# Performance work log

Measured on AMD Instinct MI355X. Metric: run time of the kernel, lower is better.

Reference implementation:

```python
import jax, jax.numpy as jnp
import numpy as np

B, T = 16, 1024
EMBED, HIDDEN = 128, 256
NUM_CLASSES, NUM_LABELS = 8000, 100


def setup_inputs() -> dict:
    key = jax.random.key(0)
    ks = jax.random.split(key, 9)
    s_in = 1.0 / np.sqrt(HIDDEN)  # PyTorch LSTMCell init: U(-1/sqrt(H), 1/sqrt(H))
    return {
        "x": jax.random.randint(ks[0], (B, T, 2), 0, NUM_LABELS, dtype=jnp.int64),
        "embed_x_w": jax.random.uniform(ks[1], (NUM_CLASSES, EMBED), jnp.float32, -0.1, 0.1),
        "embed_label_w": jax.random.uniform(ks[2], (NUM_LABELS, EMBED), jnp.float32, -0.1, 0.1),
        "W_ih": jax.random.uniform(ks[3], (4 * HIDDEN, 2 * EMBED), jnp.float32, -s_in, s_in),
        "W_hh": jax.random.uniform(ks[4], (4 * HIDDEN, HIDDEN), jnp.float32, -s_in, s_in),
        "b_ih": jax.random.uniform(ks[5], (4 * HIDDEN,), jnp.float32, -s_in, s_in),
        "b_hh": jax.random.uniform(ks[6], (4 * HIDDEN,), jnp.float32, -s_in, s_in),
        "fc_w": jax.random.uniform(ks[7], (NUM_CLASSES, HIDDEN), jnp.float32, -s_in, s_in),
        "fc_b": jax.random.uniform(ks[8], (NUM_CLASSES,), jnp.float32, -s_in, s_in),
    }


def _lstm_forward(x, embed_x_w, embed_label_w, W_ih, W_hh, b_ih, b_hh, fc_w, fc_b):
    H = W_hh.shape[1]
    # embedding lookups + concat: [B, T, 2E]
    x_emb = embed_x_w[x[:, :, 0]]
    l_emb = embed_label_w[x[:, :, 1]]
    inp = jnp.concatenate([x_emb, l_emb], axis=-1)
    # precompute input projection for all timesteps: [T, B, 4H]
    x_proj = jnp.einsum("bte,ge->tbg", inp, W_ih) + b_ih + b_hh

    def step(carry, xp_t):
        h, c = carry
        gates = xp_t + h @ W_hh.T  # [B, 4H]
        i = jax.nn.sigmoid(gates[:, 0 * H:1 * H])
        f = jax.nn.sigmoid(gates[:, 1 * H:2 * H])
        g = jnp.tanh(gates[:, 2 * H:3 * H])
        o = jax.nn.sigmoid(gates[:, 3 * H:4 * H])
        c_new = f * c + i * g
        h_new = o * jnp.tanh(c_new)
        return (h_new, c_new), h_new

    bsz = x.shape[0]
    h0 = jnp.zeros((bsz, H), x_proj.dtype)
    c0 = jnp.zeros((bsz, H), x_proj.dtype)
    _, hs = jax.lax.scan(step, (h0, c0), x_proj)  # hs: [T, B, H]
    hs = jnp.transpose(hs, (1, 0, 2))  # [B, T, H]
    return jnp.einsum("bth,ch->btc", hs, fc_w) + fc_b  # [B, T, C]


def reference(x, embed_x_w, embed_label_w, W_ih, W_hh, b_ih, b_hh, fc_w, fc_b):
    return _lstm_forward(x, embed_x_w, embed_label_w, W_ih, W_hh, b_ih, b_hh, fc_w, fc_b)
```

## Files before the change

kernel.cpp:

```cpp
#include <hip/hip_runtime.h>
#include <hip/hip_bf16.h>
#include <stdint.h>

#define B_ 16
#define T_ 1024
#define EMBED_ 128
#define HID_ 256
#define G4_ 1024
#define NC_ 8000
#define M_ (B_*T_)

typedef short bf16x8 __attribute__((ext_vector_type(8)));
typedef float f32x4 __attribute__((ext_vector_type(4)));

#if defined(__has_builtin)
#if __has_builtin(__builtin_amdgcn_sdot4)
#define SDOT4(a,b,c) __builtin_amdgcn_sdot4((a),(b),(c),false)
#endif
#endif
#ifndef SDOT4
__device__ __forceinline__ int sdot4_sw(int a, int b, int c) {
    c += (int)(signed char)(a)       * (int)(signed char)(b);
    c += (int)(signed char)(a >> 8)  * (int)(signed char)(b >> 8);
    c += (int)(signed char)(a >> 16) * (int)(signed char)(b >> 16);
    c += (int)(signed char)(a >> 24) * (int)(signed char)(b >> 24);
    return c;
}
#define SDOT4(a,b,c) sdot4_sw((a),(b),(c))
#endif

__device__ __forceinline__ float sigmoid_f(float x) {
    float e = __expf(-x);
    return __builtin_amdgcn_rcpf(1.f + e);
}

__global__ void embed_kernel(const int* __restrict__ x,
                             const float* __restrict__ ew,
                             const float* __restrict__ lw,
                             __hip_bfloat16* __restrict__ inp) {
    int m = blockIdx.x;
    int e = threadIdx.x;
    int i0 = x[2 * m];
    int i1 = x[2 * m + 1];
    float v = (e < EMBED_) ? ew[i0 * EMBED_ + e] : lw[i1 * EMBED_ + (e - EMBED_)];
    inp[m * 256 + e] = __float2bfloat16(v);
}

__global__ void f2bf_kernel(const float* __restrict__ in,
                            __hip_bfloat16* __restrict__ out, int n) {
    int i = blockIdx.x * blockDim.x + threadIdx.x;
    if (i < n) out[i] = __float2bfloat16(in[i]);
}

__global__ void quant_whh_kernel(const float* __restrict__ whh,
                                 int* __restrict__ wq, float* __restrict__ wscale) {
    int r = blockIdx.x;
    int lane = threadIdx.x;
    float4 v = ((const float4*)(whh + r * HID_))[lane];
    float m = fmaxf(fmaxf(fabsf(v.x), fabsf(v.y)), fmaxf(fabsf(v.z), fabsf(v.w)));
    #pragma unroll
    for (int off = 32; off; off >>= 1) m = fmaxf(m, __shfl_xor(m, off, 64));
    m = fmaxf(m, 1e-20f);
    float inv = 127.f / m;
    int q0 = __float2int_rn(v.x * inv) & 255;
    int q1 = __float2int_rn(v.y * inv) & 255;
    int q2 = __float2int_rn(v.z * inv) & 255;
    int q3 = __float2int_rn(v.w * inv) & 255;
    wq[r * 64 + lane] = q0 | (q1 << 8) | (q2 << 16) | (q3 << 24);
    if (lane == 0) wscale[r] = m * (1.f / 127.f);
}

__global__ __launch_bounds__(256, 4)
void gemm_bf16_kernel(const __hip_bfloat16* __restrict__ A,
                      const __hip_bfloat16* __restrict__ Bm,
                      const float* __restrict__ bias1,
                      const float* __restrict__ bias2,
                      float* __restrict__ C,
                      int N, int out_mode) {
    __shared__ short As[64][136];
    __shared__ short Bs[64][136];
    const int tid = threadIdx.x;
    const int m0 = blockIdx.y * 64;
    const int n0 = blockIdx.x * 64;
    const int w = tid >> 6;
    const int lane = tid & 63;
    const int l15 = lane & 15;
    const int q = lane >> 4;

    f32x4 zero4 = {0.f, 0.f, 0.f, 0.f};
    f32x4 acc[4] = {zero4, zero4, zero4, zero4};

    const int r = tid >> 2;
    const int cbase = tid & 3;

    for (int ko = 0; ko < 256; ko += 128) {
        #pragma unroll
        for (int i = 0; i < 4; ++i) {
            int c = cbase + (i << 2);
            uint4 av = ((const uint4*)A)[(size_t)(m0 + r) * 32 + (ko >> 3) + c];
            *((uint4*)&As[r][c * 8]) = av;
            uint4 bv = ((const uint4*)Bm)[(size_t)(n0 + r) * 32 + (ko >> 3) + c];
            *((uint4*)&Bs[r][c * 8]) = bv;
        }
        __syncthreads();
        #pragma unroll
        for (int kc = 0; kc < 4; ++kc) {
            bf16x8 af = *((const bf16x8*)&As[w * 16 + l15][kc * 32 + q * 8]);
            #pragma unroll
            for (int nt = 0; nt < 4; ++nt) {
                bf16x8 bfr = *((const bf16x8*)&Bs[nt * 16 + l15][kc * 32 + q * 8]);
                acc[nt] = __builtin_amdgcn_mfma_f32_16x16x32_bf16(af, bfr, acc[nt], 0, 0, 0);
            }
        }
        __syncthreads();
    }

    #pragma unroll
    for (int nt = 0; nt < 4; ++nt) {
        int n = n0 + nt * 16 + l15;
        float bsum = bias1[n] + (bias2 ? bias2[n] : 0.f);
        #pragma unroll
        for (int rg = 0; rg < 4; ++rg) {
            int m = m0 + w * 16 + q * 4 + rg;
            float val = acc[nt][rg] + bsum;
            if (out_mode == 0) {
                C[(size_t)m * N + n] = val;
            } else {
                int t = m & (T_ - 1), b = m >> 10;
                C[((size_t)((t << 4) + b) << 10) + n] = val;
            }
        }
    }
}

__global__ __launch_bounds__(512, 2)
void lstm_scan_kernel(const int* __restrict__ wq,
                      const float* __restrict__ wscale,
                      const float* __restrict__ xproj,
                      __hip_bfloat16* __restrict__ hs) {
    __shared__ __align__(16) int h_lds[2][64];

    const int tid = threadIdx.x;
    const int b = blockIdx.x;
    const int u = tid >> 1;
    const int odd = tid & 1;
    const int r0 = odd ? (256 + u) : u;
    const int r1 = odd ? (768 + u) : (512 + u);

    int w0[64], w1[64];
    {
        const int4* p0 = (const int4*)wq + r0 * 16;
        const int4* p1 = (const int4*)wq + r1 * 16;
        #pragma unroll
        for (int i = 0; i < 16; ++i) {
            int4 a = p0[i];
            w0[4 * i + 0] = a.x; w0[4 * i + 1] = a.y; w0[4 * i + 2] = a.z; w0[4 * i + 3] = a.w;
            int4 bb = p1[i];
            w1[4 * i + 0] = bb.x; w1[4 * i + 1] = bb.y; w1[4 * i + 2] = bb.z; w1[4 * i + 3] = bb.w;
        }
    }
    const float qs0 = wscale[r0] * (1.f / 127.f);
    const float qs1 = wscale[r1] * (1.f / 127.f);
    const float kb = odd ? 1.f : 2.f;
    const float mb = odd ? 1.f : 2.f;
    const float nb = odd ? 0.f : -1.f;

    if (tid < 64) h_lds[0][tid] = 0;
    float c = 0.f;
    float xp0 = xproj[(b << 10) + r0];
    float xp1 = xproj[(b << 10) + r1];
    __syncthreads();

    for (int t = 0; t < T_; ++t) {
        float nx0 = 0.f, nx1 = 0.f;
        if (t < T_ - 1) {
            const float* p = xproj + ((size_t)(((t + 1) << 4) + b) << 10);
            nx0 = p[r0];
            nx1 = p[r1];
        }
        int acc0 = 0, acc1 = 0;
        const int* hb = h_lds[t & 1];
        #pragma unroll
        for (int kd = 0; kd < 16; ++kd) {
            int4 hv = *((const int4*)(hb + kd * 4));
            acc0 = SDOT4(w0[4 * kd + 0], hv.x, acc0);
            acc0 = SDOT4(w0[4 * kd + 1], hv.y, acc0);
            acc0 = SDOT4(w0[4 * kd + 2], hv.z, acc0);
            acc0 = SDOT4(w0[4 * kd + 3], hv.w, acc0);
            acc1 = SDOT4(w1[4 * kd + 0], hv.x, acc1);
            acc1 = SDOT4(w1[4 * kd + 1], hv.y, acc1);
            acc1 = SDOT4(w1[4 * kd + 2], hv.z, acc1);
            acc1 = SDOT4(w1[4 * kd + 3], hv.w, acc1);
        }
        float ga = (float)acc0 * qs0 + xp0;
        float gb = (float)acc1 * qs1 + xp1;
        float a0 = sigmoid_f(ga);
        float a1 = sigmoid_f(kb * gb) * mb + nb;
        float pa0 = __shfl_xor(a0, 1, 64);
        float pa1 = __shfl_xor(a1, 1, 64);
        float iv = odd ? pa0 : a0;
        float fv = odd ? a0 : pa0;
        float gv = odd ? pa1 : a1;
        float ov = odd ? a1 : pa1;
        c = fv * c + iv * gv;
        float th = 2.f * sigmoid_f(c + c) - 1.f;
        float h = ov * th;
        if (!odd) {
            hs[(((size_t)(b << 10) + t) << 8) + u] = __float2bfloat16(h);
            ((signed char*)h_lds[(t + 1) & 1])[u] =
                (signed char)__float2int_rn(h * 127.f);
        }
        asm volatile("s_waitcnt lgkmcnt(0)" ::: "memory");
        __builtin_amdgcn_s_barrier();
        __builtin_amdgcn_sched_barrier(0);
        xp0 = nx0;
        xp1 = nx1;
    }
}

extern "C" void kernel_launch(void* const* d_in, const int* in_sizes, int n_in,
                              void* d_out, int out_size, void* d_ws, size_t ws_size,
                              hipStream_t stream) {
    const int* x            = (const int*)d_in[0];
    const float* embed_x_w  = (const float*)d_in[1];
    const float* embed_lb_w = (const float*)d_in[2];
    const float* W_ih       = (const float*)d_in[3];
    const float* W_hh       = (const float*)d_in[4];
    const float* b_ih       = (const float*)d_in[5];
    const float* b_hh       = (const float*)d_in[6];
    const float* fc_w       = (const float*)d_in[7];
    const float* fc_b       = (const float*)d_in[8];
    float* out = (float*)d_out;

    char* ws = (char*)d_ws;
    __hip_bfloat16* inp_bf = (__hip_bfloat16*)(ws);
    __hip_bfloat16* wih_bf = (__hip_bfloat16*)(ws + 8388608);
    __hip_bfloat16* fcw_bf = (__hip_bfloat16*)(ws + 8912896);
    int*   whh_q           = (int*)(ws + 13008896);
    float* whh_s           = (float*)(ws + 13271040);
    float* xproj           = (float*)(ws + 13275136);
    __hip_bfloat16* hs     = (__hip_bfloat16*)(ws + 80384000);
    (void)in_sizes; (void)n_in; (void)out_size; (void)ws_size;

    hipLaunchKernelGGL(embed_kernel, dim3(M_), dim3(256), 0, stream,
                       x, embed_x_w, embed_lb_w, inp_bf);
    hipLaunchKernelGGL(f2bf_kernel, dim3((G4_ * HID_ + 255) / 256), dim3(256), 0, stream,
                       W_ih, wih_bf, G4_ * HID_);
    hipLaunchKernelGGL(f2bf_kernel, dim3((NC_ * HID_ + 255) / 256), dim3(256), 0, stream,
                       fc_w, fcw_bf, NC_ * HID_);
    hipLaunchKernelGGL(quant_whh_kernel, dim3(G4_), dim3(64), 0, stream,
                       W_hh, whh_q, whh_s);
    hipLaunchKernelGGL(gemm_bf16_kernel, dim3(G4_ / 64, M_ / 64), dim3(256), 0, stream,
                       inp_bf, wih_bf, b_ih, b_hh, xproj, G4_, 1);
    hipLaunchKernelGGL(lstm_scan_kernel, dim3(B_), dim3(512), 0, stream,
                       whh_q, whh_s, xproj, hs);
    hipLaunchKernelGGL(gemm_bf16_kernel, dim3(NC_ / 64, M_ / 64), dim3(256), 0, stream,
                       hs, fcw_bf, fc_b, (const float*)nullptr, out, NC_, 0);
}
```

Baseline: 1.577 ms.

## Add swizzled LDS-direct FC GEMM and tighten LSTM scan inner loop

```diff
diff --git a/kernel.cpp b/kernel.cpp
--- a/kernel.cpp
+++ b/kernel.cpp
@@ -12,6 +12,7 @@
 
 typedef short bf16x8 __attribute__((ext_vector_type(8)));
 typedef float f32x4 __attribute__((ext_vector_type(4)));
+typedef unsigned int u32;
 
 #if defined(__has_builtin)
 #if __has_builtin(__builtin_amdgcn_sdot4)
@@ -33,6 +34,15 @@
     float e = __expf(-x);
     return __builtin_amdgcn_rcpf(1.f + e);
 }
+
+__device__ __forceinline__ float dpp_swap1(float x) {
+    int i = __builtin_amdgcn_mov_dpp(__float_as_int(x), 0xB1, 0xF, 0xF, true);
+    return __int_as_float(i);
+}
+
+#define GLD_LDS16(gsrc, ldst) \
+    __builtin_amdgcn_global_load_lds((const __attribute__((address_space(1))) u32*)(gsrc), \
+                                     (__attribute__((address_space(3))) u32*)(ldst), 16, 0, 0)
 
 __global__ void embed_kernel(const int* __restrict__ x,
                              const float* __restrict__ ew,
@@ -133,6 +143,82 @@
     }
 }
 
+__global__ __launch_bounds__(256, 4)
+void gemm_fc_kernel(const __hip_bfloat16* __restrict__ A,
+                    const __hip_bfloat16* __restrict__ Bm,
+                    const float* __restrict__ bias,
+                    float* __restrict__ C) {
+    __shared__ __align__(16) short As[128 * 64];
+    __shared__ __align__(16) short Bs[64 * 64];
+    const int tid  = threadIdx.x;
+    const int wid  = tid >> 6;
+    const int lane = tid & 63;
+    const int m0 = blockIdx.y * 128;
+    const int n0 = blockIdx.x * 64;
+    const int l15 = lane & 15;
+    const int q = lane >> 4;
+
+    f32x4 zero4 = {0.f, 0.f, 0.f, 0.f};
+    f32x4 acc[2][4];
+    #pragma unroll
+    for (int mf = 0; mf < 2; ++mf)
+        #pragma unroll
+        for (int nf = 0; nf < 4; ++nf) acc[mf][nf] = zero4;
+
+    const int srow = (wid << 3) + (lane >> 3);
+    const int scl  = (lane & 7) << 4;
+
+    for (int ko = 0; ko < 256; ko += 64) {
+        #pragma unroll
+        for (int is = 0; is < 4; ++is) {
+            int row = (is << 5) + srow;
+            int cb  = scl ^ ((row & 7) << 4);
+            const char* gp = (const char*)(A + (size_t)(m0 + row) * 256) + ko * 2 + cb;
+            char* lp = (char*)As + (is << 12) + (wid << 10);
+            GLD_LDS16(gp, lp);
+        }
+        #pragma unroll
+        for (int is = 0; is < 2; ++is) {
+            int row = (is << 5) + srow;
+            int cb  = scl ^ ((row & 7) << 4);
+            const char* gp = (const char*)(Bm + (size_t)(n0 + row) * 256) + ko * 2 + cb;
+            char* lp = (char*)Bs + (is << 12) + (wid << 10);
+            GLD_LDS16(gp, lp);
+        }
+        __syncthreads();
+        #pragma unroll
+        for (int kc = 0; kc < 2; ++kc) {
+            const int kb = kc * 64 + q * 16;
+            #pragma unroll
+            for (int mf = 0; mf < 2; ++mf) {
+                const int ar = (wid << 5) + mf * 16 + l15;
+                bf16x8 af = *(const bf16x8*)((const char*)As + ar * 128 + (kb ^ ((ar & 7) << 4)));
+                #pragma unroll
+                for (int nf = 0; nf < 4; ++nf) {
+                    const int br = nf * 16 + l15;
+                    bf16x8 bf = *(const bf16x8*)((const char*)Bs + br * 128 + (kb ^ ((br & 7) << 4)));
+                    acc[mf][nf] = __builtin_amdgcn_mfma_f32_16x16x32_bf16(af, bf, acc[mf][nf], 0, 0, 0);
+                }
+            }
+        }
+        __syncthreads();
+    }
+
+    #pragma unroll
+    for (int nf = 0; nf < 4; ++nf) {
+        int n = n0 + nf * 16 + l15;
+        float bs = bias[n];
+        #pragma unroll
+        for (int mf = 0; mf < 2; ++mf) {
+            #pragma unroll
+            for (int rg = 0; rg < 4; ++rg) {
+                int m = m0 + (wid << 5) + mf * 16 + q * 4 + rg;
+                C[(size_t)m * NC_ + n] = acc[mf][nf][rg] + bs;
+            }
+        }
+    }
+}
+
 __global__ __launch_bounds__(512, 2)
 void lstm_scan_kernel(const int* __restrict__ wq,
                       const float* __restrict__ wscale,
@@ -178,26 +264,40 @@
             nx0 = p[r0];
             nx1 = p[r1];
         }
-        int acc0 = 0, acc1 = 0;
-        const int* hb = h_lds[t & 1];
-        #pragma unroll
-        for (int kd = 0; kd < 16; ++kd) {
-            int4 hv = *((const int4*)(hb + kd * 4));
-            acc0 = SDOT4(w0[4 * kd + 0], hv.x, acc0);
-            acc0 = SDOT4(w0[4 * kd + 1], hv.y, acc0);
-            acc0 = SDOT4(w0[4 * kd + 2], hv.z, acc0);
-            acc0 = SDOT4(w0[4 * kd + 3], hv.w, acc0);
-            acc1 = SDOT4(w1[4 * kd + 0], hv.x, acc1);
-            acc1 = SDOT4(w1[4 * kd + 1], hv.y, acc1);
-            acc1 = SDOT4(w1[4 * kd + 2], hv.z, acc1);
-            acc1 = SDOT4(w1[4 * kd + 3], hv.w, acc1);
-        }
-        float ga = (float)acc0 * qs0 + xp0;
-        float gb = (float)acc1 * qs1 + xp1;
+        const int4* hb = (const int4*)h_lds[t & 1];
+        int4 hv[16];
+        #pragma unroll
+        for (int i = 0; i < 16; ++i) hv[i] = hb[i];
+
+        int a00 = 0, a01 = 0, a10 = 0, a11 = 0;
+        #pragma unroll
+        for (int kd = 0; kd < 8; ++kd) {
+            a00 = SDOT4(w0[4 * kd + 0], hv[kd].x, a00);
+            a01 = SDOT4(w0[4 * kd + 1], hv[kd].y, a01);
+            a00 = SDOT4(w0[4 * kd + 2], hv[kd].z, a00);
+            a01 = SDOT4(w0[4 * kd + 3], hv[kd].w, a01);
+            a10 = SDOT4(w1[4 * kd + 0], hv[kd].x, a10);
+            a11 = SDOT4(w1[4 * kd + 1], hv[kd].y, a11);
+            a10 = SDOT4(w1[4 * kd + 2], hv[kd].z, a10);
+            a11 = SDOT4(w1[4 * kd + 3], hv[kd].w, a11);
+        }
+        #pragma unroll
+        for (int kd = 8; kd < 16; ++kd) {
+            a00 = SDOT4(w0[4 * kd + 0], hv[kd].x, a00);
+            a01 = SDOT4(w0[4 * kd + 1], hv[kd].y, a01);
+            a00 = SDOT4(w0[4 * kd + 2], hv[kd].z, a00);
+            a01 = SDOT4(w0[4 * kd + 3], hv[kd].w, a01);
+            a10 = SDOT4(w1[4 * kd + 0], hv[kd].x, a10);
+            a11 = SDOT4(w1[4 * kd + 1], hv[kd].y, a11);
+            a10 = SDOT4(w1[4 * kd + 2], hv[kd].z, a10);
+            a11 = SDOT4(w1[4 * kd + 3], hv[kd].w, a11);
+        }
+        float ga = (float)(a00 + a01) * qs0 + xp0;
+        float gb = (float)(a10 + a11) * qs1 + xp1;
         float a0 = sigmoid_f(ga);
         float a1 = sigmoid_f(kb * gb) * mb + nb;
-        float pa0 = __shfl_xor(a0, 1, 64);
-        float pa1 = __shfl_xor(a1, 1, 64);
+        float pa0 = dpp_swap1(a0);
+        float pa1 = dpp_swap1(a1);
         float iv = odd ? pa0 : a0;
         float fv = odd ? a0 : pa0;
         float gv = odd ? pa1 : a1;
@@ -206,13 +306,12 @@
         float th = 2.f * sigmoid_f(c + c) - 1.f;
         float h = ov * th;
         if (!odd) {
-            hs[(((size_t)(b << 10) + t) << 8) + u] = __float2bfloat16(h);
             ((signed char*)h_lds[(t + 1) & 1])[u] =
                 (signed char)__float2int_rn(h * 127.f);
+            hs[(((size_t)(b << 10) + t) << 8) + u] = __float2bfloat16(h);
         }
         asm volatile("s_waitcnt lgkmcnt(0)" ::: "memory");
         __builtin_amdgcn_s_barrier();
-        __builtin_amdgcn_sched_barrier(0);
         xp0 = nx0;
         xp1 = nx1;
     }
@@ -254,6 +353,6 @@
                        inp_bf, wih_bf, b_ih, b_hh, xproj, G4_, 1);
     hipLaunchKernelGGL(lstm_scan_kernel, dim3(B_), dim3(512), 0, stream,
                        whh_q, whh_s, xproj, hs);
-    hipLaunchKernelGGL(gemm_bf16_kernel, dim3(NC_ / 64, M_ / 64), dim3(256), 0, stream,
-                       hs, fcw_bf, fc_b, (const float*)nullptr, out, NC_, 0);
-}
+    hipLaunchKernelGGL(gemm_fc_kernel, dim3(NC_ / 64, M_ / 128), dim3(256), 0, stream,
+                       hs, fcw_bf, fc_b, out);
+}
```

After: 1.431 ms. 9.3% less time.
